# Performance work log

Hardware: AMD Instinct MI355X
Metric: run time of the kernel (lower is better)

## Reference

```python
import jax, jax.numpy as jnp
import numpy as np

D_MODEL = 1024
N_HEADS = 16
HEAD_DIM = D_MODEL // N_HEADS  # 64, rope_dim == head_dim
D_FF = 4096
BATCH = 2
SEQ = 2048
EPS = 1e-6


def setup_inputs() -> dict:
    key = jax.random.key(0)
    ks = jax.random.split(key, 12)
    x = jax.random.normal(ks[0], (BATCH, SEQ, D_MODEL), dtype=jnp.float32)
    # realistic RoPE angles: theta = pos * inv_freq, duplicated to fill rope_dim
    half = HEAD_DIM // 2
    inv_freq = 1.0 / (10000.0 ** (jnp.arange(0, half, dtype=jnp.float32) / half))
    pos = jnp.arange(SEQ, dtype=jnp.float32)
    freqs = pos[:, None] * inv_freq[None, :]              # [S, half]
    rotary_pos_emb = jnp.concatenate([freqs, freqs], axis=-1)[:, None, :]  # [S,1,64]
    s = D_MODEL ** -0.5
    wq = jax.random.normal(ks[1], (D_MODEL, D_MODEL), dtype=jnp.float32) * s
    wk = jax.random.normal(ks[2], (D_MODEL, D_MODEL), dtype=jnp.float32) * s
    wv = jax.random.normal(ks[3], (D_MODEL, D_MODEL), dtype=jnp.float32) * s
    wo = jax.random.normal(ks[4], (D_MODEL, D_MODEL), dtype=jnp.float32) * s
    w_gate = jax.random.normal(ks[5], (D_FF, D_MODEL), dtype=jnp.float32) * s
    w_up = jax.random.normal(ks[6], (D_FF, D_MODEL), dtype=jnp.float32) * s
    w_down = jax.random.normal(ks[7], (D_MODEL, D_FF), dtype=jnp.float32) * (D_FF ** -0.5)
    norm1_w = jnp.ones((D_MODEL,), dtype=jnp.float32)
    norm2_w = jnp.ones((D_MODEL,), dtype=jnp.float32)
    return {"x": x, "rotary_pos_emb": rotary_pos_emb, "wq": wq, "wk": wk,
            "wv": wv, "wo": wo, "w_gate": w_gate, "w_up": w_up,
            "w_down": w_down, "norm1_w": norm1_w, "norm2_w": norm2_w}


def _rms_norm(x, w):
    # torch: x / (||x||/sqrt(d) + eps) * w  (eps added to the norm, not variance)
    norm = jnp.linalg.norm(x, axis=-1, keepdims=True) * (x.shape[-1] ** -0.5)
    return x / (norm + EPS) * w


def _rotate_half(t):
    t1, t2 = jnp.split(t, 2, axis=-1)
    return jnp.concatenate([-t2, t1], axis=-1)


def _apply_rope(t, cos, sin):
    # t: [B,H,S,D]; cos/sin: [S,D] broadcast over batch/heads
    return t * cos[None, None] + _rotate_half(t) * sin[None, None]


def reference(x, rotary_pos_emb, wq, wk, wv, wo, w_gate, w_up, w_down, norm1_w, norm2_w):
    B, S, _ = x.shape
    H, D = N_HEADS, HEAD_DIM

    # ---- attention sublayer ----
    residual = x
    h = _rms_norm(x, norm1_w)
    q = (h @ wq.T).reshape(B, S, H, D).transpose(0, 2, 1, 3)  # [B,H,S,D]
    k = (h @ wk.T).reshape(B, S, H, D).transpose(0, 2, 1, 3)
    v = (h @ wv.T).reshape(B, S, H, D).transpose(0, 2, 1, 3)

    freqs = rotary_pos_emb[:, 0, :]  # [S, D] (rope_dim == head_dim)
    cos, sin = jnp.cos(freqs), jnp.sin(freqs)
    q = _apply_rope(q, cos, sin)
    k = _apply_rope(k, cos, sin)

    scores = jnp.einsum('bhsd,bhtd->bhst', q, k) / jnp.sqrt(jnp.float32(D))
    causal = jnp.tril(jnp.ones((S, S), dtype=bool))  # True = keep
    scores = jnp.where(causal[None, None], scores, jnp.finfo(scores.dtype).min)
    attn = jax.nn.softmax(scores, axis=-1)  # dropout is identity in eval
    attn_out = jnp.einsum('bhst,bhtd->bhsd', attn, v)
    attn_out = attn_out.transpose(0, 2, 1, 3).reshape(B, S, H * D)
    x = residual + attn_out @ wo.T

    # ---- SwiGLU MLP sublayer ----
    residual = x
    h = _rms_norm(x, norm2_w)
    gate = h @ w_gate.T
    up = h @ w_up.T
    ff = (jax.nn.silu(gate) * up) @ w_down.T
    return residual + ff
```

## Files before the change

kernel.cpp:

```cpp
#include <hip/hip_runtime.h>

typedef __bf16 bf16;
typedef __attribute__((ext_vector_type(8))) __bf16 bf16x8;
typedef __attribute__((ext_vector_type(4))) float f32x4;

#define B_SZ 2
#define SEQ 2048
#define DM 1024
#define NH 16
#define HD 64
#define DFF 4096
#define NROWS (B_SZ*SEQ)

#define QSCALE 0.18033688f
#define DEFER_THR 11.541561f

__device__ __forceinline__ f32x4 mfma16(bf16x8 a, bf16x8 b, f32x4 c) {
    return __builtin_amdgcn_mfma_f32_16x16x32_bf16(a, b, c, 0, 0, 0);
}

__device__ __forceinline__ void gload16(const bf16* g, bf16* l) {
    __builtin_amdgcn_global_load_lds(
        (const __attribute__((address_space(1))) void*)g,
        (__attribute__((address_space(3))) void*)l, 16, 0, 0);
}


__global__ __launch_bounds__(256) void convert_all_k(
    const float* __restrict__ wq, const float* __restrict__ wk,
    const float* __restrict__ wv, const float* __restrict__ wo,
    const float* __restrict__ wg, const float* __restrict__ wu,
    const float* __restrict__ wd,
    bf16* __restrict__ wqkvb, bf16* __restrict__ wob,
    bf16* __restrict__ wgub, bf16* __restrict__ wdb) {
    const long M1 = 1l << 20;
    long i = ((long)blockIdx.x * 256 + threadIdx.x) * 8;
    const float* src; bf16* dst; long off;
    if (i < 3 * M1) {
        int sct = (int)(i >> 20);
        src = sct == 0 ? wq : (sct == 1 ? wk : wv);
        off = i & (M1 - 1); dst = wqkvb + i;
    } else if (i < 4 * M1) {
        src = wo; off = i - 3 * M1; dst = wob + off;
    } else if (i < 12 * M1) {
        long j = i - 4 * M1;
        int fr = (int)(j >> 10), c = (int)(j & 1023);
        int g = fr >> 6, r = fr & 63;
        int f = g * 32 + (r & 31);
        src = (r & 32) ? wu : wg; off = (long)f * 1024 + c; dst = wgub + j;
    } else {
        src = wd; off = i - 12 * M1; dst = wdb + off;
    }
    float4 v0 = *(const float4*)(src + off);
    float4 v1 = *(const float4*)(src + off + 4);
    dst[0] = (bf16)v0.x; dst[1] = (bf16)v0.y; dst[2] = (bf16)v0.z; dst[3] = (bf16)v0.w;
    dst[4] = (bf16)v1.x; dst[5] = (bf16)v1.y; dst[6] = (bf16)v1.z; dst[7] = (bf16)v1.w;
}

__global__ __launch_bounds__(256) void rope_table_k(const float* __restrict__ rope,
                                                    float* __restrict__ ct,
                                                    float* __restrict__ st) {
    int i = blockIdx.x * 256 + threadIdx.x;
    int sI = i >> 5, d = i & 31;
    float f = rope[sI * 64 + d];
    ct[i] = cosf(f);
    st[i] = sinf(f);
}

__global__ __launch_bounds__(256) void rmsnorm_k(const float* __restrict__ x,
                                                 const float* __restrict__ w,
                                                 bf16* __restrict__ o) {
    const int wv = threadIdx.x >> 6, l = threadIdx.x & 63;
    const long row = (long)blockIdx.x * 4 + wv;
    const float4* xr = (const float4*)(x + row * DM);
    float4 v[4];
    float ss = 0.f;
    #pragma unroll
    for (int j = 0; j < 4; ++j) {
        v[j] = xr[l + j * 64];
        ss += v[j].x*v[j].x + v[j].y*v[j].y + v[j].z*v[j].z + v[j].w*v[j].w;
    }
    #pragma unroll
    for (int off = 32; off >= 1; off >>= 1) ss += __shfl_xor(ss, off, 64);
    float scale = 1.f / (sqrtf(ss * (1.f / (float)DM)) + 1e-6f);
    bf16* orow = o + row * DM;
    #pragma unroll
    for (int j = 0; j < 4; ++j) {
        float4 wv4 = ((const float4*)w)[l + j * 64];
        bf16 t[4];
        t[0] = (bf16)(v[j].x * scale * wv4.x);
        t[1] = (bf16)(v[j].y * scale * wv4.y);
        t[2] = (bf16)(v[j].z * scale * wv4.z);
        t[3] = (bf16)(v[j].w * scale * wv4.w);
        *(short4*)(orow + (l + j * 64) * 4) = *(short4*)t;
    }
}


template<int EPI>
__global__ __launch_bounds__(512, 2)
void gemm256(const bf16* __restrict__ A, const bf16* __restrict__ W,
             int K, bf16* __restrict__ o1, bf16* __restrict__ o2,
             bf16* __restrict__ o3,
             const float* __restrict__ ct, const float* __restrict__ st) {
    __shared__ __align__(16) char smem[131072];
    bf16* Ah = (bf16*)smem;
    bf16* Bh = (bf16*)(smem + 65536);
    const int tid = threadIdx.x;
    const int wid = tid >> 6, l = tid & 63;
    const int lr = l & 15, lg = l >> 4;
    const int wr = wid >> 2, wcn = wid & 3;
    const int nwg = gridDim.x * gridDim.y;
    const int orig = blockIdx.y * gridDim.x + blockIdx.x;
    const int swz = (orig & 7) * (nwg >> 3) + (orig >> 3);
    const int bx = swz % gridDim.x, by = swz / gridDim.x;
    const long mbase = (long)bx * 256;
    const long nbase = (long)by * 256;

    f32x4 acc[8][4] = {};
    const int nk = K >> 6;
    const int P = nk * 2;

    const int aoff0 = lr * 64 + ((wr * 4 + lg) ^ (lr & 7)) * 8;
    const int boff0 = ((wcn & 1) * 64 + lr) * 64 + (((wcn >> 1) * 4 + lg) ^ (lr & 7)) * 8;

    auto stageHalf = [&](int ph) {
        const int buf = ph & 3, h = ph & 1, kt = ph >> 1;
        bf16* abase = Ah + buf * 8192;
        bf16* bbase = Bh + buf * 8192;
        const long kcol = (long)kt * 64 + h * 32;
        #pragma unroll
        for (int i = 0; i < 2; ++i) {
            int s = i * 512 + tid;
            int prow = s >> 3, pblk = s & 7;
            int L = pblk ^ (prow & 7);
            long gr = (long)((L >> 2) * 128 + prow);
            long gc = kcol + (L & 3) * 8;
            gload16(&A[(mbase + gr) * K + gc], abase + s * 8);
            gload16(&W[(nbase + gr) * K + gc], bbase + s * 8);
        }
    };

    auto computeHalf = [&](int ph) {
        const int buf = ph & 3;
        const bf16* abase = Ah + buf * 8192;
        const bf16* bbase = Bh + buf * 8192;
        bf16x8 bfr[4];
        #pragma unroll
        for (int ni = 0; ni < 4; ++ni)
            bfr[ni] = *(const bf16x8*)&bbase[ni * 1024 + boff0];
        #pragma unroll
        for (int ms = 0; ms < 2; ++ms) {
            bf16x8 af[4];
            #pragma unroll
            for (int mi = 0; mi < 4; ++mi)
                af[mi] = *(const bf16x8*)&abase[(ms * 4 + mi) * 1024 + aoff0];
            __builtin_amdgcn_s_setprio(1);
            #pragma unroll
            for (int mi = 0; mi < 4; ++mi)
                #pragma unroll
                for (int ni = 0; ni < 4; ++ni)
                    acc[ms * 4 + mi][ni] = mfma16(af[mi], bfr[ni], acc[ms * 4 + mi][ni]);
            __builtin_amdgcn_s_setprio(0);
        }
    };

    stageHalf(0);
    stageHalf(1);
    stageHalf(2);
    for (int p = 0; p < P; ++p) {
        if (p < P - 2)       asm volatile("s_waitcnt vmcnt(8)" ::: "memory");
        else if (p == P - 2) asm volatile("s_waitcnt vmcnt(4)" ::: "memory");
        else                 asm volatile("s_waitcnt vmcnt(0)" ::: "memory");
        __builtin_amdgcn_s_barrier();
        __builtin_amdgcn_sched_barrier(0);
        if (p + 3 < P) stageHalf(p + 3);
        computeHalf(p);
    }

    if (EPI == 0) {
        const long colW = nbase + wcn * 64;
        const int sect = (int)(colW >> 10);
        const int hh = (int)((colW >> 6) & 15);
        #pragma unroll
        for (int a = 0; a < 8; ++a) {
            #pragma unroll
            for (int nn = 0; nn < 2; ++nn) {
                const int dd = nn * 16 + lr;
                #pragma unroll
                for (int r = 0; r < 4; ++r) {
                    long row = mbase + wr * 128 + a * 16 + 4 * lg + r;
                    int b = (int)(row >> 11), s = (int)(row & 2047);
                    float v1 = acc[a][nn][r];
                    float v2 = acc[a][nn + 2][r];
                    if (sect < 2) {
                        if (sect == 0) { v1 *= QSCALE; v2 *= QSCALE; }
                        float c = ct[s * 32 + dd], sn = st[s * 32 + dd];
                        bf16* dst = (sect == 0) ? o1 : o2;
                        long pth = (((long)(b * NH + hh) * SEQ + s) << 6) + dd;
                        dst[pth]      = (bf16)(v1 * c - v2 * sn);
                        dst[pth + 32] = (bf16)(v2 * c + v1 * sn);
                    } else {
                        long pth = ((long)(b * NH + hh) * HD + dd) * SEQ + s;
                        o3[pth]            = (bf16)v1;
                        o3[pth + 32 * SEQ] = (bf16)v2;
                    }
                }
            }
        }
    }

    if (EPI == 3) {
        const int fb = (int)(nbase + wcn * 64) >> 1;
        #pragma unroll
        for (int a = 0; a < 8; ++a)
            #pragma unroll
            for (int ni = 0; ni < 2; ++ni)
                #pragma unroll
                for (int r = 0; r < 4; ++r) {
                    long row = mbase + wr * 128 + a * 16 + 4 * lg + r;
                    float g = acc[a][ni][r];
                    float u = acc[a][ni + 2][r];
                    float sg = g / (1.f + __expf(-g));
                    o1[row * 4096 + fb + ni * 16 + lr] = (bf16)(sg * u);
                }
    }
}


__global__ __launch_bounds__(512, 4)
void gemm64x128(const bf16* __restrict__ A, const bf16* __restrict__ W,
                int K, int N, const float* __restrict__ resid, float* __restrict__ of) {
    __shared__ bf16 As[3][64 * 64];
    __shared__ bf16 Bs[3][128 * 64];
    const int tid = threadIdx.x;
    const int wid = tid >> 6, l = tid & 63;
    const int lr = l & 15, lg = l >> 4;
    const int wr = wid >> 2, wcn = wid & 3;
    const long mbase = (long)blockIdx.x * 64;
    const long nbase = (long)blockIdx.y * 128;

    f32x4 acc[2][2] = {};
    const int nk = K >> 6;

    auto stage = [&](int b, int kt) {
        {
            int s = tid;
            int row = s >> 3, pblk = s & 7;
            int L = pblk ^ (row & 7);
            gload16(&A[(mbase + row) * K + kt * 64 + L * 8], &As[b][s * 8]);
        }
        #pragma unroll
        for (int i = 0; i < 2; ++i) {
            int s = i * 512 + tid;
            int row = s >> 3, pblk = s & 7;
            int L = pblk ^ (row & 7);
            gload16(&W[(nbase + row) * K + kt * 64 + L * 8], &Bs[b][s * 8]);
        }
    };
    auto compute = [&](int b) {
        #pragma unroll
        for (int kk = 0; kk < 2; ++kk) {
            bf16x8 af[2], bfr[2];
            #pragma unroll
            for (int mi = 0; mi < 2; ++mi) {
                int row = wr * 32 + mi * 16 + lr;
                af[mi] = *(const bf16x8*)&As[b][row * 64 + ((kk * 4 + lg) ^ (lr & 7)) * 8];
            }
            #pragma unroll
            for (int ni = 0; ni < 2; ++ni) {
                int row = wcn * 32 + ni * 16 + lr;
                bfr[ni] = *(const bf16x8*)&Bs[b][row * 64 + ((kk * 4 + lg) ^ (lr & 7)) * 8];
            }
            __builtin_amdgcn_s_setprio(1);
            #pragma unroll
            for (int mi = 0; mi < 2; ++mi)
                #pragma unroll
                for (int ni = 0; ni < 2; ++ni)
                    acc[mi][ni] = mfma16(af[mi], bfr[ni], acc[mi][ni]);
            __builtin_amdgcn_s_setprio(0);
        }
    };

    stage(0, 0);
    stage(1, 1);
    for (int kt = 0; kt < nk; ++kt) {
        if (kt < nk - 1) asm volatile("s_waitcnt vmcnt(3)" ::: "memory");
        else             asm volatile("s_waitcnt vmcnt(0)" ::: "memory");
        __builtin_amdgcn_s_barrier();
        __builtin_amdgcn_sched_barrier(0);
        if (kt + 2 < nk) stage((kt + 2) % 3, kt + 2);
        compute(kt % 3);
    }

    #pragma unroll
    for (int mi = 0; mi < 2; ++mi)
        #pragma unroll
        for (int ni = 0; ni < 2; ++ni)
            #pragma unroll
            for (int r = 0; r < 4; ++r) {
                long row = mbase + wr * 32 + mi * 16 + 4 * lg + r;
                long col = nbase + wcn * 32 + ni * 16 + lr;
                of[row * N + col] = resid[row * N + col] + acc[mi][ni][r];
            }
}


__device__ __forceinline__ void attn_tile(
    int tb, int qw, bool diag,
    const bf16x8& qf0, const bf16x8& qf1,
    const bf16* Kl, const bf16* Vl, bf16* Plw,
    int lr, int lg, f32x4* oacc, float* mr, f32x4& lacc)
{
    f32x4 s[4];
    __builtin_amdgcn_s_setprio(1);
    #pragma unroll
    for (int tf = 0; tf < 4; ++tf) {
        f32x4 z = {0.f, 0.f, 0.f, 0.f};
        bf16x8 k0 = *(const bf16x8*)&Kl[(tf * 16 + lr) * 64 + ((0 + lg) ^ (lr & 7)) * 8];
        bf16x8 k1 = *(const bf16x8*)&Kl[(tf * 16 + lr) * 64 + ((4 + lg) ^ (lr & 7)) * 8];
        z = mfma16(qf0, k0, z);
        z = mfma16(qf1, k1, z);
        s[tf] = z;
    }
    __builtin_amdgcn_s_setprio(0);

    float pv[4][4];
    float pml[4];
    #pragma unroll
    for (int r = 0; r < 4; ++r) pml[r] = -1e30f;
    #pragma unroll
    for (int tf = 0; tf < 4; ++tf) {
        int t = tb + tf * 16 + lr;
        #pragma unroll
        for (int r = 0; r < 4; ++r) {
            float sv = s[tf][r];
            if (diag && t > qw + 4 * lg + r) sv = -1e30f;
            pv[tf][r] = sv;
            pml[r] = fmaxf(pml[r], sv);
        }
    }
    bool ok = (pml[0] <= mr[0] + DEFER_THR) && (pml[1] <= mr[1] + DEFER_THR) &&
              (pml[2] <= mr[2] + DEFER_THR) && (pml[3] <= mr[3] + DEFER_THR);
    if (!__all(ok)) {
        float pmax[4];
        #pragma unroll
        for (int r = 0; r < 4; ++r) {
            pmax[r] = pml[r];
            pmax[r] = fmaxf(pmax[r], __shfl_xor(pmax[r], 8, 64));
            pmax[r] = fmaxf(pmax[r], __shfl_xor(pmax[r], 4, 64));
            pmax[r] = fmaxf(pmax[r], __shfl_xor(pmax[r], 2, 64));
            pmax[r] = fmaxf(pmax[r], __shfl_xor(pmax[r], 1, 64));
        }
        float alpha[4];
        #pragma unroll
        for (int r = 0; r < 4; ++r) {
            float mn = fmaxf(mr[r], pmax[r]);
            alpha[r] = exp2f(mr[r] - mn);
            mr[r] = mn;
        }
        #pragma unroll
        for (int r = 0; r < 4; ++r) lacc[r] *= alpha[r];
        #pragma unroll
        for (int df = 0; df < 4; ++df) {
            f32x4 t4 = oacc[df];
            t4[0] *= alpha[0]; t4[1] *= alpha[1];
            t4[2] *= alpha[2]; t4[3] *= alpha[3];
            oacc[df] = t4;
        }
    }
    #pragma unroll
    for (int tf = 0; tf < 4; ++tf)
        #pragma unroll
        for (int r = 0; r < 4; ++r)
            Plw[(4 * lg + r) * 72 + tf * 16 + lr] = (bf16)exp2f(pv[tf][r] - mr[r]);

    bf16x8 pa0 = *(const bf16x8*)&Plw[lr * 72 + lg * 8];
    bf16x8 pa1 = *(const bf16x8*)&Plw[lr * 72 + 32 + lg * 8];
    bf16x8 ones;
    #pragma unroll
    for (int j = 0; j < 8; ++j) ones[j] = (bf16)1.0f;
    __builtin_amdgcn_s_setprio(1);
    lacc = mfma16(pa0, ones, lacc);
    lacc = mfma16(pa1, ones, lacc);
    #pragma unroll
    for (int df = 0; df < 4; ++df) {
        bf16x8 v0 = *(const bf16x8*)&Vl[(df * 16 + lr) * 64 + ((0 + lg) ^ (lr & 7)) * 8];
        bf16x8 v1 = *(const bf16x8*)&Vl[(df * 16 + lr) * 64 + ((4 + lg) ^ (lr & 7)) * 8];
        oacc[df] = mfma16(pa0, v0, oacc[df]);
        oacc[df] = mfma16(pa1, v1, oacc[df]);
    }
    __builtin_amdgcn_s_setprio(0);
}

__global__ __launch_bounds__(256)
void attn_fwd(const bf16* __restrict__ q, const bf16* __restrict__ k,
              const bf16* __restrict__ vt, bf16* __restrict__ o) {
    __shared__ bf16 Kl[2][64 * 64];
    __shared__ bf16 Vl[2][64 * 64];
    __shared__ bf16 Pl[4][16 * 72];
    const int tid = threadIdx.x, wid = tid >> 6, l = tid & 63;
    const int lr = l & 15, lg = l >> 4;
    const int qtA = blockIdx.x;
    const int qtB = 31 - qtA;
    const int bh = blockIdx.y;
    const long kbase = (long)bh * SEQ * HD;
    const long vbase = (long)bh * HD * SEQ;
    const int qwA = qtA * 64 + wid * 16;
    const int qwB = qtB * 64 + wid * 16;

    bf16x8 qA0, qA1, qB0, qB1;
    {
        const bf16* qp = q + kbase + (long)(qwA + lr) * HD + lg * 8;
        qA0 = *(const bf16x8*)qp; qA1 = *(const bf16x8*)(qp + 32);
        const bf16* qp2 = q + kbase + (long)(qwB + lr) * HD + lg * 8;
        qB0 = *(const bf16x8*)qp2; qB1 = *(const bf16x8*)(qp2 + 32);
    }
    f32x4 oA[4] = {}, oB[4] = {};
    f32x4 lA = {0.f, 0.f, 0.f, 0.f}, lB = {0.f, 0.f, 0.f, 0.f};
    float mA[4] = {-1e30f, -1e30f, -1e30f, -1e30f};
    float mB[4] = {-1e30f, -1e30f, -1e30f, -1e30f};

    auto stageKV = [&](int b, int tb) {
        #pragma unroll
        for (int i = 0; i < 4; ++i) {
            int slot = i * 256 + tid;
            int row = (slot >> 3) & 63;
            int bs = (slot & 7) ^ (row & 7);
            if (slot < 512)
                gload16(&k[kbase + (long)(tb + row) * HD + bs * 8], &Kl[b][slot * 8]);
            else
                gload16(&vt[vbase + (long)row * SEQ + tb + bs * 8], &Vl[b][(slot - 512) * 8]);
        }
    };

    const int nt = qtB + 1;
    stageKV(0, 0);
    __syncthreads();
    int cur = 0;
    for (int tb_i = 0; tb_i < nt; ++tb_i) {
        const int tb = tb_i * 64;
        if (tb_i + 1 < nt) stageKV(cur ^ 1, tb + 64);
        if (tb_i <= qtA)
            attn_tile(tb, qwA, tb_i == qtA, qA0, qA1, Kl[cur], Vl[cur], Pl[wid], lr, lg, oA, mA, lA);
        attn_tile(tb, qwB, tb_i == qtB, qB0, qB1, Kl[cur], Vl[cur], Pl[wid], lr, lg, oB, mB, lB);
        __syncthreads();
        cur ^= 1;
    }

    const int b = bh >> 4, h = bh & 15;
    #pragma unroll
    for (int df = 0; df < 4; ++df) {
        #pragma unroll
        for (int r = 0; r < 4; ++r) {
            int sA = qwA + 4 * lg + r;
            int sB = qwB + 4 * lg + r;
            o[((long)(b * SEQ + sA) * DM) + h * HD + df * 16 + lr] = (bf16)(oA[df][r] / lA[r]);
            o[((long)(b * SEQ + sB) * DM) + h * HD + df * 16 + lr] = (bf16)(oB[df][r] / lB[r]);
        }
    }
}


extern "C" void kernel_launch(void* const* d_in, const int* in_sizes, int n_in,
                              void* d_out, int out_size, void* d_ws, size_t ws_size,
                              hipStream_t stream) {
    (void)in_sizes; (void)n_in; (void)out_size; (void)ws_size;
    const float* x    = (const float*)d_in[0];
    const float* rope = (const float*)d_in[1];
    const float* wq   = (const float*)d_in[2];
    const float* wk   = (const float*)d_in[3];
    const float* wv   = (const float*)d_in[4];
    const float* wo   = (const float*)d_in[5];
    const float* wg   = (const float*)d_in[6];
    const float* wu   = (const float*)d_in[7];
    const float* wd   = (const float*)d_in[8];
    const float* n1w  = (const float*)d_in[9];
    const float* n2w  = (const float*)d_in[10];
    float* out = (float*)d_out;

    char* ws = (char*)d_ws;
    const size_t MB = 1u << 20;
    bf16* wqkvb = (bf16*)(ws + 0 * MB);
    bf16* wob   = (bf16*)(ws + 6 * MB);
    bf16* wgub  = (bf16*)(ws + 8 * MB);
    bf16* wdb   = (bf16*)(ws + 24 * MB);
    bf16* hb    = (bf16*)(ws + 32 * MB);
    bf16* qb_   = (bf16*)(ws + 40 * MB);
    bf16* kb_   = (bf16*)(ws + 56 * MB);
    bf16* vtb   = (bf16*)(ws + 72 * MB);
    bf16* attnb = (bf16*)(ws + 88 * MB);
    float* x2   = (float*)(ws + 40 * MB);
    bf16* midb  = (bf16*)(ws + 56 * MB);
    float* ctab = (float*)(ws + 104 * MB);
    float* stab = (float*)(ws + 104 * MB + (1u << 18));

    convert_all_k<<<8192, 256, 0, stream>>>(wq, wk, wv, wo, wg, wu, wd,
                                            wqkvb, wob, wgub, wdb);
    rope_table_k<<<256, 256, 0, stream>>>(rope, ctab, stab);

    rmsnorm_k<<<NROWS / 4, 256, 0, stream>>>(x, n1w, hb);

    gemm256<0><<<dim3(16, 12), 512, 0, stream>>>(hb, wqkvb, DM, qb_, kb_, vtb, ctab, stab);

    attn_fwd<<<dim3(16, 32), 256, 0, stream>>>(qb_, kb_, vtb, attnb);

    gemm64x128<<<dim3(64, 8), 512, 0, stream>>>(attnb, wob, DM, DM, x, x2);

    rmsnorm_k<<<NROWS / 4, 256, 0, stream>>>(x2, n2w, hb);

    gemm256<3><<<dim3(16, 32), 512, 0, stream>>>(hb, wgub, DM, midb, nullptr, nullptr, nullptr, nullptr);

    gemm64x128<<<dim3(64, 8), 512, 0, stream>>>(midb, wdb, DFF, DM, x2, out);
}
```

Baseline: 285.0 us.

## Restructure 64x128 GEMM to 4 waves, 32-wide K steps with 4-deep pipeline

Rewrites the output-projection and down-projection GEMM kernel to use 256 threads (4 waves, each computing a 32x64 subtile) instead of 512 threads with 32x32 subtiles. The K loop now steps by 32 with a 4-buffer LDS ring and three stages in flight, using a new XOR swizzle for 32-element rows. The aim is more MFMA work per LDS fragment load, better register reuse and deeper prefetch to hide global latency, at the cost of fewer waves per block and more barriers per unit of K.

```diff
diff --git a/kernel.cpp b/kernel.cpp
--- a/kernel.cpp
+++ b/kernel.cpp
@@ -228,79 +228,78 @@
 }
 
 
-__global__ __launch_bounds__(512, 4)
+__global__ __launch_bounds__(256, 2)
 void gemm64x128(const bf16* __restrict__ A, const bf16* __restrict__ W,
                 int K, int N, const float* __restrict__ resid, float* __restrict__ of) {
-    __shared__ bf16 As[3][64 * 64];
-    __shared__ bf16 Bs[3][128 * 64];
+    __shared__ __align__(16) bf16 Ah[4][64 * 32];
+    __shared__ __align__(16) bf16 Bh[4][128 * 32];
     const int tid = threadIdx.x;
     const int wid = tid >> 6, l = tid & 63;
     const int lr = l & 15, lg = l >> 4;
-    const int wr = wid >> 2, wcn = wid & 3;
+    const int wr = wid >> 1, wcn = wid & 1;
     const long mbase = (long)blockIdx.x * 64;
     const long nbase = (long)blockIdx.y * 128;
 
-    f32x4 acc[2][2] = {};
-    const int nk = K >> 6;
-
-    auto stage = [&](int b, int kt) {
+    f32x4 acc[2][4] = {};
+    const int P = K >> 5;
+
+    const int rchunk = (lg ^ (lr & 3) ^ ((lr >> 2) & 3)) * 8;
+
+    auto stage = [&](int p) {
+        const int buf = p & 3;
+        const long kcol = (long)p * 32;
         {
-            int s = tid;
-            int row = s >> 3, pblk = s & 7;
-            int L = pblk ^ (row & 7);
-            gload16(&A[(mbase + row) * K + kt * 64 + L * 8], &As[b][s * 8]);
+            int row = tid >> 2, pblk = tid & 3;
+            int L = pblk ^ (row & 3) ^ ((row >> 2) & 3);
+            gload16(&A[(mbase + row) * K + kcol + L * 8], &Ah[buf][tid * 8]);
         }
         #pragma unroll
         for (int i = 0; i < 2; ++i) {
-            int s = i * 512 + tid;
-            int row = s >> 3, pblk = s & 7;
-            int L = pblk ^ (row & 7);
-            gload16(&W[(nbase + row) * K + kt * 64 + L * 8], &Bs[b][s * 8]);
+            int s = i * 256 + tid;
+            int row = s >> 2, pblk = s & 3;
+            int L = pblk ^ (row & 3) ^ ((row >> 2) & 3);
+            gload16(&W[(nbase + row) * K + kcol + L * 8], &Bh[buf][s * 8]);
         }
     };
-    auto compute = [&](int b) {
-        #pragma unroll
-        for (int kk = 0; kk < 2; ++kk) {
-            bf16x8 af[2], bfr[2];
+    auto compute = [&](int p) {
+        const int buf = p & 3;
+        bf16x8 af[2], bfr[4];
+        #pragma unroll
+        for (int mi = 0; mi < 2; ++mi)
+            af[mi] = *(const bf16x8*)&Ah[buf][(wr * 32 + mi * 16 + lr) * 32 + rchunk];
+        #pragma unroll
+        for (int ni = 0; ni < 4; ++ni)
+            bfr[ni] = *(const bf16x8*)&Bh[buf][(wcn * 64 + ni * 16 + lr) * 32 + rchunk];
+        __builtin_amdgcn_s_setprio(1);
+        #pragma unroll
+        for (int mi = 0; mi < 2; ++mi)
             #pragma unroll
-            for (int mi = 0; mi < 2; ++mi) {
-                int row = wr * 32 + mi * 16 + lr;
-                af[mi] = *(const bf16x8*)&As[b][row * 64 + ((kk * 4 + lg) ^ (lr & 7)) * 8];
-            }
-            #pragma unroll
-            for (int ni = 0; ni < 2; ++ni) {
-                int row = wcn * 32 + ni * 16 + lr;
-                bfr[ni] = *(const bf16x8*)&Bs[b][row * 64 + ((kk * 4 + lg) ^ (lr & 7)) * 8];
-            }
-            __builtin_amdgcn_s_setprio(1);
-            #pragma unroll
-            for (int mi = 0; mi < 2; ++mi)
-                #pragma unroll
-                for (int ni = 0; ni < 2; ++ni)
-                    acc[mi][ni] = mfma16(af[mi], bfr[ni], acc[mi][ni]);
-            __builtin_amdgcn_s_setprio(0);
-        }
+            for (int ni = 0; ni < 4; ++ni)
+                acc[mi][ni] = mfma16(af[mi], bfr[ni], acc[mi][ni]);
+        __builtin_amdgcn_s_setprio(0);
     };
 
-    stage(0, 0);
-    stage(1, 1);
-    for (int kt = 0; kt < nk; ++kt) {
-        if (kt < nk - 1) asm volatile("s_waitcnt vmcnt(3)" ::: "memory");
-        else             asm volatile("s_waitcnt vmcnt(0)" ::: "memory");
+    stage(0);
+    stage(1);
+    stage(2);
+    for (int p = 0; p < P; ++p) {
+        if (p < P - 2)       asm volatile("s_waitcnt vmcnt(6)" ::: "memory");
+        else if (p == P - 2) asm volatile("s_waitcnt vmcnt(3)" ::: "memory");
+        else                 asm volatile("s_waitcnt vmcnt(0)" ::: "memory");
         __builtin_amdgcn_s_barrier();
         __builtin_amdgcn_sched_barrier(0);
-        if (kt + 2 < nk) stage((kt + 2) % 3, kt + 2);
-        compute(kt % 3);
+        if (p + 3 < P) stage(p + 3);
+        compute(p);
     }
 
     #pragma unroll
     for (int mi = 0; mi < 2; ++mi)
         #pragma unroll
-        for (int ni = 0; ni < 2; ++ni)
+        for (int ni = 0; ni < 4; ++ni)
             #pragma unroll
             for (int r = 0; r < 4; ++r) {
                 long row = mbase + wr * 32 + mi * 16 + 4 * lg + r;
-                long col = nbase + wcn * 32 + ni * 16 + lr;
+                long col = nbase + wcn * 64 + ni * 16 + lr;
                 of[row * N + col] = resid[row * N + col] + acc[mi][ni][r];
             }
 }
@@ -505,11 +504,11 @@
 
     attn_fwd<<<dim3(16, 32), 256, 0, stream>>>(qb_, kb_, vtb, attnb);
 
-    gemm64x128<<<dim3(64, 8), 512, 0, stream>>>(attnb, wob, DM, DM, x, x2);
+    gemm64x128<<<dim3(64, 8), 256, 0, stream>>>(attnb, wob, DM, DM, x, x2);
 
     rmsnorm_k<<<NROWS / 4, 256, 0, stream>>>(x2, n2w, hb);
 
     gemm256<3><<<dim3(16, 32), 512, 0, stream>>>(hb, wgub, DM, midb, nullptr, nullptr, nullptr, nullptr);
 
-    gemm64x128<<<dim3(64, 8), 512, 0, stream>>>(midb, wdb, DFF, DM, x2, out);
-}
+    gemm64x128<<<dim3(64, 8), 256, 0, stream>>>(midb, wdb, DFF, DM, x2, out);
+}
```

After: 303.2 us. 1.06x slower.

## Use 128-row query tiles with 8 waves and triple-buffered KV pipeline in attention

Applied to the files above, without the earlier changes.

The attention kernel now runs 512 threads per block, each block covering two 128-row query tiles (8 waves of 16 rows) instead of two 64-row tiles, so each staged K/V tile is shared by twice as many waves. K/V staging moves from double to triple buffering with explicit vmcnt waits and a single barrier per iteration, prefetching two tiles ahead. The aim is to cut global K/V traffic per query and hide load latency better, at the cost of more LDS per block, fewer blocks (256 instead of 512), and per-wave causal diagonal handling.

```diff
diff --git a/kernel.cpp b/kernel.cpp
--- a/kernel.cpp
+++ b/kernel.cpp
@@ -393,21 +393,24 @@
     __builtin_amdgcn_s_setprio(0);
 }
 
-__global__ __launch_bounds__(256)
+__global__ __launch_bounds__(512)
 void attn_fwd(const bf16* __restrict__ q, const bf16* __restrict__ k,
               const bf16* __restrict__ vt, bf16* __restrict__ o) {
-    __shared__ bf16 Kl[2][64 * 64];
-    __shared__ bf16 Vl[2][64 * 64];
-    __shared__ bf16 Pl[4][16 * 72];
+    __shared__ bf16 Kl[3][64 * 64];
+    __shared__ bf16 Vl[3][64 * 64];
+    __shared__ bf16 Pl[8][16 * 72];
     const int tid = threadIdx.x, wid = tid >> 6, l = tid & 63;
     const int lr = l & 15, lg = l >> 4;
-    const int qtA = blockIdx.x;
-    const int qtB = 31 - qtA;
+    const int stA = blockIdx.x;
+    const int stB = 15 - stA;
     const int bh = blockIdx.y;
     const long kbase = (long)bh * SEQ * HD;
     const long vbase = (long)bh * HD * SEQ;
-    const int qwA = qtA * 64 + wid * 16;
-    const int qwB = qtB * 64 + wid * 16;
+    const int qwA = stA * 128 + wid * 16;
+    const int qwB = stB * 128 + wid * 16;
+    const int dA = 2 * stA + (wid >> 2);
+    const int dB = 2 * stB + (wid >> 2);
+    const int nt = 2 * stB + 2;
 
     bf16x8 qA0, qA1, qB0, qB1;
     {
@@ -423,8 +426,8 @@
 
     auto stageKV = [&](int b, int tb) {
         #pragma unroll
-        for (int i = 0; i < 4; ++i) {
-            int slot = i * 256 + tid;
+        for (int i = 0; i < 2; ++i) {
+            int slot = i * 512 + tid;
             int row = (slot >> 3) & 63;
             int bs = (slot & 7) ^ (row & 7);
             if (slot < 512)
@@ -434,18 +437,20 @@
         }
     };
 
-    const int nt = qtB + 1;
     stageKV(0, 0);
-    __syncthreads();
-    int cur = 0;
-    for (int tb_i = 0; tb_i < nt; ++tb_i) {
-        const int tb = tb_i * 64;
-        if (tb_i + 1 < nt) stageKV(cur ^ 1, tb + 64);
-        if (tb_i <= qtA)
-            attn_tile(tb, qwA, tb_i == qtA, qA0, qA1, Kl[cur], Vl[cur], Pl[wid], lr, lg, oA, mA, lA);
-        attn_tile(tb, qwB, tb_i == qtB, qB0, qB1, Kl[cur], Vl[cur], Pl[wid], lr, lg, oB, mB, lB);
-        __syncthreads();
-        cur ^= 1;
+    stageKV(1, 64);
+    for (int p = 0; p < nt; ++p) {
+        if (p < nt - 1) asm volatile("s_waitcnt vmcnt(2)" ::: "memory");
+        else            asm volatile("s_waitcnt vmcnt(0)" ::: "memory");
+        __builtin_amdgcn_s_barrier();
+        __builtin_amdgcn_sched_barrier(0);
+        if (p + 2 < nt) stageKV((p + 2) % 3, (p + 2) * 64);
+        const int tb = p * 64;
+        const int buf = p % 3;
+        if (p <= dA)
+            attn_tile(tb, qwA, p == dA, qA0, qA1, Kl[buf], Vl[buf], Pl[wid], lr, lg, oA, mA, lA);
+        if (p <= dB)
+            attn_tile(tb, qwB, p == dB, qB0, qB1, Kl[buf], Vl[buf], Pl[wid], lr, lg, oB, mB, lB);
     }
 
     const int b = bh >> 4, h = bh & 15;
@@ -503,7 +508,7 @@
 
     gemm256<0><<<dim3(16, 12), 512, 0, stream>>>(hb, wqkvb, DM, qb_, kb_, vtb, ctab, stab);
 
-    attn_fwd<<<dim3(16, 32), 256, 0, stream>>>(qb_, kb_, vtb, attnb);
+    attn_fwd<<<dim3(8, 32), 512, 0, stream>>>(qb_, kb_, vtb, attnb);
 
     gemm64x128<<<dim3(64, 8), 512, 0, stream>>>(attnb, wob, DM, DM, x, x2);
 
```

After: 287.9 us. Within noise of the previous version (+1.0%).
